# Optimization experiments

Measured on AMD Instinct MI355X. Metric: run time of the kernel, lower is better.

The kernel has to match this reference:

```python
import jax, jax.numpy as jnp
import numpy as np

B, SORB, H, L = 32768, 64, 256, 2


def setup_inputs() -> dict:
    key = jax.random.key(0)
    ks = jax.random.split(key, 11)
    s = 1.0 / np.sqrt(H)

    def u(k, shape):
        return jax.random.uniform(k, shape, jnp.float32, -s, s)

    return {
        "x": jax.random.randint(ks[0], (B, SORB), 0, 2).astype(jnp.int32),
        # PyTorch GRU params, gate order (r, z, n); layer 0 input_size=2, layer 1 input_size=H
        "w_ih0": u(ks[1], (3 * H, 2)), "w_hh0": u(ks[2], (3 * H, H)),
        "b_ih0": u(ks[3], (3 * H,)), "b_hh0": u(ks[4], (3 * H,)),
        "w_ih1": u(ks[5], (3 * H, H)), "w_hh1": u(ks[6], (3 * H, H)),
        "b_ih1": u(ks[7], (3 * H,)), "b_hh1": u(ks[8], (3 * H,)),
        "w_amp": u(ks[9], (2, H)), "b_amp": u(ks[10], (2,)),
    }


def _gru_cell(x, h, w_ih, w_hh, b_ih, b_hh):
    # PyTorch GRUCell math, gates in (r, z, n) order
    gi = x @ w_ih.T + b_ih
    gh = h @ w_hh.T + b_hh
    ir, iz, i_n = jnp.split(gi, 3, axis=-1)
    hr, hz, h_n = jnp.split(gh, 3, axis=-1)
    r = jax.nn.sigmoid(ir + hr)
    z = jax.nn.sigmoid(iz + hz)
    n = jnp.tanh(i_n + r * h_n)
    return (1.0 - z) * n + z * h


def reference(x, w_ih0, w_hh0, b_ih0, b_hh0, w_ih1, w_hh1, b_ih1, b_hh1, w_amp, b_amp):
    bits = x  # [B, SORB], values in {0,1} (equals ((+-1)+1)/2 of original input)
    nb = bits.shape[0]
    layer_params = [(w_ih0, w_hh0, b_ih0, b_hh0), (w_ih1, w_hh1, b_ih1, b_hh1)]

    def stacked(inp, h):  # h: [L, B, H]
        hs = []
        for l, (wi, wh, bi, bh) in enumerate(layer_params):
            hl = _gru_cell(inp, h[l], wi, wh, bi, bh)
            hs.append(hl)
            inp = hl
        return inp, jnp.stack(hs)

    h0 = jnp.zeros((L, nb, H), jnp.float32)
    # priming step with zero input (x0 = zeros(nbatch,1,2))
    _, h = stacked(jnp.zeros((nb, 2), jnp.float32), h0)

    def step(h, b_t):  # b_t: [B]
        onehot = jax.nn.one_hot(b_t, 2, dtype=jnp.float32)
        y, h = stacked(onehot, h)
        amp = jax.nn.softmax(y @ w_amp.T + b_amp, axis=1)  # [B, 2]
        p = jnp.sum(amp * onehot, axis=1)  # conditional prob of the sampled bit
        return h, p

    _, probs = jax.lax.scan(step, h, bits.T)  # probs: [SORB, B]
    return jnp.sqrt(jnp.prod(probs, axis=0))  # wavefunction amplitude, [B]
```

## Files before the change

kernel.cpp:

```cpp
#include <hip/hip_runtime.h>

typedef _Float16 f16;
typedef _Float16 f16x8 __attribute__((ext_vector_type(8)));
typedef float f32x4 __attribute__((ext_vector_type(4)));

#define H_    256
#define TB_   64
#define NT_   1024
#define SORB_ 64
#define SLOT_ 8192

#define MFMA16(a, b, c) __builtin_amdgcn_mfma_f32_16x16x32_f16((a), (b), (c), 0, 0, 0)
#define UNR _Pragma("unroll")

__device__ __forceinline__ float sigm(float v) {
  return __builtin_amdgcn_rcpf(1.0f + __builtin_amdgcn_exp2f(v * -1.442695040888963f));
}
__device__ __forceinline__ float tanh_fast(float v) {
  float a = fabsf(v);
  float e = __builtin_amdgcn_exp2f(a * -2.885390081777927f);
  float t = (1.0f - e) * __builtin_amdgcn_rcpf(1.0f + e);
  return copysignf(t, v);
}
__device__ __forceinline__ int lswz(int lrow, int col) {
  return lrow * H_ + (col ^ ((lrow & 7) << 3));
}

__global__ void wcvt(const float* __restrict__ a, const float* __restrict__ b,
                     const float* __restrict__ c, f16* __restrict__ o) {
  int i = blockIdx.x * 256 + threadIdx.x;
  const int n = 768 * 256;
  if (i < n) {
    o[i]         = (f16)a[i];
    o[n + i]     = (f16)b[i];
    o[2 * n + i] = (f16)c[i];
  }
}

__global__ __launch_bounds__(NT_, 4) void rnnwf(
    const int* __restrict__ x,
    const float* __restrict__ w_ih0, const float* __restrict__ b_ih0,
    const float* __restrict__ b_hh0, const float* __restrict__ b_ih1,
    const float* __restrict__ b_hh1, const float* __restrict__ w_amp,
    const float* __restrict__ b_amp, const f16* __restrict__ W16,
    float* __restrict__ out)
{
  __shared__ __align__(16) f16 hall[8 * SLOT_];
  __shared__ float wampL[512];
  __shared__ __align__(8) unsigned short bitsL[TB_ * 4];
  __shared__ unsigned long long bitsT[SORB_];

  const int tid  = threadIdx.x;
  const int wave = tid >> 6;
  const int lane = tid & 63;
  const int l15  = lane & 15;
  const int lg   = lane >> 4;
  const int lg4  = lg << 2;
  const int col  = wave * 16 + l15;
  const int rowbase = blockIdx.x * TB_;

  for (int j = tid; j < 512; j += NT_) wampL[j] = w_amp[j];
  if (tid < TB_ * 4) {
    const int* xp = x + (size_t)(rowbase + (tid >> 2)) * SORB_ + (tid & 3) * 16;
    unsigned m = 0;
    #pragma unroll
    for (int i = 0; i < 16; ++i) m |= (unsigned)(xp[i] & 1) << i;
    bitsL[tid] = (unsigned short)m;
  }
  for (int i = tid; i < 8 * SLOT_; i += NT_) hall[i] = (f16)0.f;
  __syncthreads();
  if (tid < SORB_) {
    unsigned long long mkk = 0ull;
    const int q = tid >> 4, sh = tid & 15;
    #pragma unroll 4
    for (int r = 0; r < TB_; ++r)
      mkk |= (unsigned long long)((bitsL[r * 4 + q] >> sh) & 1) << r;
    bitsT[tid] = mkk;
  }
  const int hrow = tid >> 4;
  const int t16  = tid & 15;
  const unsigned long long hmk = ((const unsigned long long*)bitsL)[hrow];

  const float baseR = b_ih0[col]       + b_hh0[col];
  const float baseZ = b_ih0[256 + col] + b_hh0[256 + col];
  const float baseN = b_ih0[512 + col];
  const float sumR0 = baseR + w_ih0[2 * col + 0],         dR = w_ih0[2 * col + 1] - w_ih0[2 * col + 0];
  const float sumZ0 = baseZ + w_ih0[2 * (256 + col) + 0], dZ = w_ih0[2 * (256 + col) + 1] - w_ih0[2 * (256 + col) + 0];
  const float sumN0 = baseN + w_ih0[2 * (512 + col) + 0], dN = w_ih0[2 * (512 + col) + 1] - w_ih0[2 * (512 + col) + 0];
  const float bhh0n_c = b_hh0[512 + col];
  const float b1r_c   = b_ih1[col]       + b_hh1[col];
  const float b1z_c   = b_ih1[256 + col] + b_hh1[256 + col];
  const float b1ni_c  = b_ih1[512 + col];
  const float b1nh_c  = b_hh1[512 + col];
  const float ba0 = b_amp[0], ba1 = b_amp[1];
  __syncthreads();

  float prob = 1.0f;
  const f16* p0base = W16 + col * 256;
  const f16* pibase = W16 + 768 * 256 + col * 256;
  const f16* phbase = W16 + 2 * 768 * 256 + col * 256;

  for (int tau = -1; tau <= 64; ++tau) {
    const int h0r = ((tau + 1) & 1) * (2 * SLOT_);
    const int h0w = (tau & 1) * (2 * SLOT_);
    const int h1r = 4 * SLOT_ + ((tau + 1) & 1) * (2 * SLOT_);
    const int h1w = 4 * SLOT_ + (tau & 1) * (2 * SLOT_);
    const bool doS = (tau < 64), doT = (tau >= 0);

    unsigned lo32 = 0u, hi32 = 0u;
    if (tau >= 0 && tau < 64) {
      unsigned long long mkk = bitsT[tau];
      lo32 = (unsigned)mkk; hi32 = (unsigned)(mkk >> 32);
    }

    f32x4 aR0[4], aZ0[4], aN0[4], tR[4], tZ[4];
    UNR for (int m = 0; m < 4; ++m) {
      aR0[m] = (f32x4){0,0,0,0}; aZ0[m] = aR0[m]; aN0[m] = aR0[m];
      tR[m] = aR0[m]; tZ[m] = aR0[m];
    }
    #pragma unroll 2
    for (int kt = 0; kt < 8; ++kt) {
      const int k0 = kt * 32 + lg * 8;
      f16x8 A0[4];
      UNR for (int m = 0; m < 4; ++m)
        A0[m] = *(const f16x8*)&hall[h0r + (m >> 1) * SLOT_ + lswz((m & 1) * 16 + l15, k0)];
      if (doS) {
        f16x8 Br = *(const f16x8*)(p0base + k0);
        f16x8 Bz = *(const f16x8*)(p0base + 65536 + k0);
        f16x8 Bn = *(const f16x8*)(p0base + 131072 + k0);
        UNR for (int m = 0; m < 4; ++m) {
          aR0[m] = MFMA16(A0[m], Br, aR0[m]);
          aZ0[m] = MFMA16(A0[m], Bz, aZ0[m]);
          aN0[m] = MFMA16(A0[m], Bn, aN0[m]);
        }
      }
      if (doT) {
        f16x8 BiR = *(const f16x8*)(pibase + k0);
        f16x8 BiZ = *(const f16x8*)(pibase + 65536 + k0);
        f16x8 BhR = *(const f16x8*)(phbase + k0);
        f16x8 BhZ = *(const f16x8*)(phbase + 65536 + k0);
        f16x8 A1[4];
        UNR for (int m = 0; m < 4; ++m)
          A1[m] = *(const f16x8*)&hall[h1r + (m >> 1) * SLOT_ + lswz((m & 1) * 16 + l15, k0)];
        UNR for (int m = 0; m < 4; ++m) {
          tR[m] = MFMA16(A0[m], BiR, tR[m]);  tR[m] = MFMA16(A1[m], BhR, tR[m]);
          tZ[m] = MFMA16(A0[m], BiZ, tZ[m]);  tZ[m] = MFMA16(A1[m], BhZ, tZ[m]);
        }
      }
    }
    f32x4 rv[4], zv[4];
    if (doT) {
      UNR for (int m = 0; m < 4; ++m)
        UNR for (int e = 0; e < 4; ++e) {
          rv[m][e] = sigm(tR[m][e] + b1r_c);
          zv[m][e] = sigm(tZ[m][e] + b1z_c);
        }
    }

    f32x4 tNi[4], tNh[4];
    UNR for (int m = 0; m < 4; ++m) { tNi[m] = (f32x4){0,0,0,0}; tNh[m] = tNi[m]; }
    if (doT) {
      #pragma unroll 2
      for (int kt = 0; kt < 8; ++kt) {
        const int k0 = kt * 32 + lg * 8;
        f16x8 BiN = *(const f16x8*)(pibase + 131072 + k0);
        f16x8 BhN = *(const f16x8*)(phbase + 131072 + k0);
        UNR for (int m = 0; m < 4; ++m) {
          f16x8 A0 = *(const f16x8*)&hall[h0r + (m >> 1) * SLOT_ + lswz((m & 1) * 16 + l15, k0)];
          f16x8 A1 = *(const f16x8*)&hall[h1r + (m >> 1) * SLOT_ + lswz((m & 1) * 16 + l15, k0)];
          tNi[m] = MFMA16(A0, BiN, tNi[m]);
          tNh[m] = MFMA16(A1, BhN, tNh[m]);
        }
      }
    }

    if (doS) {
      if (tau >= 0) {
        UNR for (int m = 0; m < 4; ++m) {
          const unsigned hsel = (m < 2) ? lo32 : hi32;
          UNR for (int e = 0; e < 4; ++e) {
            const int lrow = (m & 1) * 16 + lg4 + e;
            float fb = (float)((hsel >> ((m & 1) * 16 + lg4 + e)) & 1u);
            float giR = fmaf(fb, dR, sumR0);
            float giZ = fmaf(fb, dZ, sumZ0);
            float giN = fmaf(fb, dN, sumN0);
            float r  = sigm(aR0[m][e] + giR);
            float z  = sigm(aZ0[m][e] + giZ);
            float n  = tanh_fast(giN + r * (aN0[m][e] + bhh0n_c));
            float ho = (float)hall[h0r + (m >> 1) * SLOT_ + lswz(lrow, col)];
            hall[h0w + (m >> 1) * SLOT_ + lswz(lrow, col)] = (f16)((1.0f - z) * n + z * ho);
          }
        }
      } else {
        UNR for (int m = 0; m < 4; ++m) {
          UNR for (int e = 0; e < 4; ++e) {
            const int lrow = (m & 1) * 16 + lg4 + e;
            float r  = sigm(aR0[m][e] + baseR);
            float z  = sigm(aZ0[m][e] + baseZ);
            float n  = tanh_fast(baseN + r * (aN0[m][e] + bhh0n_c));
            float ho = (float)hall[h0r + (m >> 1) * SLOT_ + lswz(lrow, col)];
            hall[h0w + (m >> 1) * SLOT_ + lswz(lrow, col)] = (f16)((1.0f - z) * n + z * ho);
          }
        }
      }
    }
    if (doT) {
      UNR for (int m = 0; m < 4; ++m) {
        UNR for (int e = 0; e < 4; ++e) {
          const int lrow = (m & 1) * 16 + lg4 + e;
          float n  = tanh_fast(tNi[m][e] + b1ni_c + rv[m][e] * (tNh[m][e] + b1nh_c));
          float z  = zv[m][e];
          float ho = (float)hall[h1r + (m >> 1) * SLOT_ + lswz(lrow, col)];
          hall[h1w + (m >> 1) * SLOT_ + lswz(lrow, col)] = (f16)((1.0f - z) * n + z * ho);
        }
      }
    }
    if (tau >= 2) {
      const int t = tau - 2;
      float d0 = 0.f, d1 = 0.f;
      #pragma unroll
      for (int j = 0; j < 2; ++j) {
        const int k0 = t16 * 16 + j * 8;
        f16x8 hv = *(const f16x8*)&hall[h1r + (hrow >> 5) * SLOT_ + lswz(hrow & 31, k0)];
        f32x4 w0a = *(const f32x4*)&wampL[k0];
        f32x4 w0b = *(const f32x4*)&wampL[k0 + 4];
        f32x4 w1a = *(const f32x4*)&wampL[256 + k0];
        f32x4 w1b = *(const f32x4*)&wampL[256 + k0 + 4];
        #pragma unroll
        for (int i = 0; i < 4; ++i) {
          float hfa = (float)hv[i], hfb = (float)hv[4 + i];
          d0 = fmaf(hfa, w0a[i], d0); d0 = fmaf(hfb, w0b[i], d0);
          d1 = fmaf(hfa, w1a[i], d1); d1 = fmaf(hfb, w1b[i], d1);
        }
      }
      d0 += __shfl_xor(d0, 1); d0 += __shfl_xor(d0, 2);
      d0 += __shfl_xor(d0, 4); d0 += __shfl_xor(d0, 8);
      d1 += __shfl_xor(d1, 1); d1 += __shfl_xor(d1, 2);
      d1 += __shfl_xor(d1, 4); d1 += __shfl_xor(d1, 8);
      const int bit = (unsigned)(hmk >> t) & 1u;
      float diff = (d0 + ba0) - (d1 + ba1);
      if (bit) diff = -diff;
      prob *= __builtin_amdgcn_rcpf(1.0f + __builtin_amdgcn_exp2f(diff * -1.442695040888963f));
    }
    __syncthreads();
  }

  {
    const int hb = 4 * SLOT_;
    float d0 = 0.f, d1 = 0.f;
    #pragma unroll
    for (int j = 0; j < 2; ++j) {
      const int k0 = t16 * 16 + j * 8;
      f16x8 hv = *(const f16x8*)&hall[hb + (hrow >> 5) * SLOT_ + lswz(hrow & 31, k0)];
      f32x4 w0a = *(const f32x4*)&wampL[k0];
      f32x4 w0b = *(const f32x4*)&wampL[k0 + 4];
      f32x4 w1a = *(const f32x4*)&wampL[256 + k0];
      f32x4 w1b = *(const f32x4*)&wampL[256 + k0 + 4];
      #pragma unroll
      for (int i = 0; i < 4; ++i) {
        float hfa = (float)hv[i], hfb = (float)hv[4 + i];
        d0 = fmaf(hfa, w0a[i], d0); d0 = fmaf(hfb, w0b[i], d0);
        d1 = fmaf(hfa, w1a[i], d1); d1 = fmaf(hfb, w1b[i], d1);
      }
    }
    d0 += __shfl_xor(d0, 1); d0 += __shfl_xor(d0, 2);
    d0 += __shfl_xor(d0, 4); d0 += __shfl_xor(d0, 8);
    d1 += __shfl_xor(d1, 1); d1 += __shfl_xor(d1, 2);
    d1 += __shfl_xor(d1, 4); d1 += __shfl_xor(d1, 8);
    const int bit = (unsigned)(hmk >> 63) & 1u;
    float diff = (d0 + ba0) - (d1 + ba1);
    if (bit) diff = -diff;
    prob *= __builtin_amdgcn_rcpf(1.0f + __builtin_amdgcn_exp2f(diff * -1.442695040888963f));
  }

  if (t16 == 0) out[rowbase + hrow] = sqrtf(prob);
}

extern "C" void kernel_launch(void* const* d_in, const int* in_sizes, int n_in,
                              void* d_out, int out_size, void* d_ws, size_t ws_size,
                              hipStream_t stream) {
  const int*   x     = (const int*)d_in[0];
  const float* w_ih0 = (const float*)d_in[1];
  const float* w_hh0 = (const float*)d_in[2];
  const float* b_ih0 = (const float*)d_in[3];
  const float* b_hh0 = (const float*)d_in[4];
  const float* w_ih1 = (const float*)d_in[5];
  const float* w_hh1 = (const float*)d_in[6];
  const float* b_ih1 = (const float*)d_in[7];
  const float* b_hh1 = (const float*)d_in[8];
  const float* w_amp = (const float*)d_in[9];
  const float* b_amp = (const float*)d_in[10];
  (void)in_sizes; (void)n_in; (void)out_size; (void)ws_size;

  f16* W16 = (f16*)d_ws;
  hipLaunchKernelGGL(wcvt, dim3(768), dim3(256), 0, stream, w_hh0, w_ih1, w_hh1, W16);
  hipLaunchKernelGGL(rnnwf, dim3(32768 / TB_), dim3(NT_), 0, stream,
                     x, w_ih0, b_ih0, b_hh0, b_ih1, b_hh1, w_amp, b_amp, W16,
                     (float*)d_out);
}
```

Measured before the change: 5.883 ms.

## Split fused layer GEMM loops, keep previous hidden state in registers, retune LDS swizzle

```diff
diff --git a/kernel.cpp b/kernel.cpp
--- a/kernel.cpp
+++ b/kernel.cpp
@@ -2,6 +2,7 @@
 
 typedef _Float16 f16;
 typedef _Float16 f16x8 __attribute__((ext_vector_type(8)));
+typedef _Float16 f16x4 __attribute__((ext_vector_type(4)));
 typedef float f32x4 __attribute__((ext_vector_type(4)));
 
 #define H_    256
@@ -23,7 +24,7 @@
   return copysignf(t, v);
 }
 __device__ __forceinline__ int lswz(int lrow, int col) {
-  return lrow * H_ + (col ^ ((lrow & 7) << 3));
+  return lrow * H_ + (col ^ (((lrow ^ (lrow >> 2)) & 7) << 3));
 }
 
 __global__ void wcvt(const float* __restrict__ a, const float* __restrict__ b,
@@ -100,12 +101,14 @@
   const f16* pibase = W16 + 768 * 256 + col * 256;
   const f16* phbase = W16 + 2 * 768 * 256 + col * 256;
 
+  f16x4 h0p[4], h1p[4];
+  UNR for (int m = 0; m < 4; ++m) { h0p[m] = (f16x4){0,0,0,0}; h1p[m] = h0p[m]; }
+
   for (int tau = -1; tau <= 64; ++tau) {
     const int h0r = ((tau + 1) & 1) * (2 * SLOT_);
     const int h0w = (tau & 1) * (2 * SLOT_);
     const int h1r = 4 * SLOT_ + ((tau + 1) & 1) * (2 * SLOT_);
     const int h1w = 4 * SLOT_ + (tau & 1) * (2 * SLOT_);
-    const bool doS = (tau < 64), doT = (tau >= 0);
 
     unsigned lo32 = 0u, hi32 = 0u;
     if (tau >= 0 && tau < 64) {
@@ -113,53 +116,31 @@
       lo32 = (unsigned)mkk; hi32 = (unsigned)(mkk >> 32);
     }
 
-    f32x4 aR0[4], aZ0[4], aN0[4], tR[4], tZ[4];
-    UNR for (int m = 0; m < 4; ++m) {
-      aR0[m] = (f32x4){0,0,0,0}; aZ0[m] = aR0[m]; aN0[m] = aR0[m];
-      tR[m] = aR0[m]; tZ[m] = aR0[m];
-    }
-    #pragma unroll 2
-    for (int kt = 0; kt < 8; ++kt) {
-      const int k0 = kt * 32 + lg * 8;
-      f16x8 A0[4];
-      UNR for (int m = 0; m < 4; ++m)
-        A0[m] = *(const f16x8*)&hall[h0r + (m >> 1) * SLOT_ + lswz((m & 1) * 16 + l15, k0)];
-      if (doS) {
-        f16x8 Br = *(const f16x8*)(p0base + k0);
-        f16x8 Bz = *(const f16x8*)(p0base + 65536 + k0);
-        f16x8 Bn = *(const f16x8*)(p0base + 131072 + k0);
-        UNR for (int m = 0; m < 4; ++m) {
-          aR0[m] = MFMA16(A0[m], Br, aR0[m]);
-          aZ0[m] = MFMA16(A0[m], Bz, aZ0[m]);
-          aN0[m] = MFMA16(A0[m], Bn, aN0[m]);
-        }
-      }
-      if (doT) {
+    if (tau >= 0) {
+      f32x4 tR[4], tZ[4];
+      UNR for (int m = 0; m < 4; ++m) { tR[m] = (f32x4){0,0,0,0}; tZ[m] = tR[m]; }
+      #pragma unroll 2
+      for (int kt = 0; kt < 8; ++kt) {
+        const int k0 = kt * 32 + lg * 8;
         f16x8 BiR = *(const f16x8*)(pibase + k0);
         f16x8 BiZ = *(const f16x8*)(pibase + 65536 + k0);
         f16x8 BhR = *(const f16x8*)(phbase + k0);
         f16x8 BhZ = *(const f16x8*)(phbase + 65536 + k0);
-        f16x8 A1[4];
-        UNR for (int m = 0; m < 4; ++m)
-          A1[m] = *(const f16x8*)&hall[h1r + (m >> 1) * SLOT_ + lswz((m & 1) * 16 + l15, k0)];
-        UNR for (int m = 0; m < 4; ++m) {
-          tR[m] = MFMA16(A0[m], BiR, tR[m]);  tR[m] = MFMA16(A1[m], BhR, tR[m]);
-          tZ[m] = MFMA16(A0[m], BiZ, tZ[m]);  tZ[m] = MFMA16(A1[m], BhZ, tZ[m]);
-        }
-      }
-    }
-    f32x4 rv[4], zv[4];
-    if (doT) {
+        UNR for (int m = 0; m < 4; ++m) {
+          f16x8 A0 = *(const f16x8*)&hall[h0r + (m >> 1) * SLOT_ + lswz((m & 1) * 16 + l15, k0)];
+          f16x8 A1 = *(const f16x8*)&hall[h1r + (m >> 1) * SLOT_ + lswz((m & 1) * 16 + l15, k0)];
+          tR[m] = MFMA16(A0, BiR, tR[m]);  tR[m] = MFMA16(A1, BhR, tR[m]);
+          tZ[m] = MFMA16(A0, BiZ, tZ[m]);  tZ[m] = MFMA16(A1, BhZ, tZ[m]);
+        }
+      }
+      f32x4 rv[4], zv[4];
       UNR for (int m = 0; m < 4; ++m)
         UNR for (int e = 0; e < 4; ++e) {
           rv[m][e] = sigm(tR[m][e] + b1r_c);
           zv[m][e] = sigm(tZ[m][e] + b1z_c);
         }
-    }
-
-    f32x4 tNi[4], tNh[4];
-    UNR for (int m = 0; m < 4; ++m) { tNi[m] = (f32x4){0,0,0,0}; tNh[m] = tNi[m]; }
-    if (doT) {
+      f32x4 tNi[4], tNh[4];
+      UNR for (int m = 0; m < 4; ++m) { tNi[m] = (f32x4){0,0,0,0}; tNh[m] = tNi[m]; }
       #pragma unroll 2
       for (int kt = 0; kt < 8; ++kt) {
         const int k0 = kt * 32 + lg * 8;
@@ -172,9 +153,34 @@
           tNh[m] = MFMA16(A1, BhN, tNh[m]);
         }
       }
-    }
-
-    if (doS) {
+      UNR for (int m = 0; m < 4; ++m) {
+        UNR for (int e = 0; e < 4; ++e) {
+          const int lrow = (m & 1) * 16 + lg4 + e;
+          float n  = tanh_fast(tNi[m][e] + b1ni_c + rv[m][e] * (tNh[m][e] + b1nh_c));
+          float z  = zv[m][e];
+          float hn = (1.0f - z) * n + z * (float)h1p[m][e];
+          h1p[m][e] = (f16)hn;
+          hall[h1w + (m >> 1) * SLOT_ + lswz(lrow, col)] = h1p[m][e];
+        }
+      }
+    }
+
+    if (tau < 64) {
+      f32x4 aR[4], aZ[4], aN[4];
+      UNR for (int m = 0; m < 4; ++m) { aR[m] = (f32x4){0,0,0,0}; aZ[m] = aR[m]; aN[m] = aR[m]; }
+      #pragma unroll 2
+      for (int kt = 0; kt < 8; ++kt) {
+        const int k0 = kt * 32 + lg * 8;
+        f16x8 Br = *(const f16x8*)(p0base + k0);
+        f16x8 Bz = *(const f16x8*)(p0base + 65536 + k0);
+        f16x8 Bn = *(const f16x8*)(p0base + 131072 + k0);
+        UNR for (int m = 0; m < 4; ++m) {
+          f16x8 A = *(const f16x8*)&hall[h0r + (m >> 1) * SLOT_ + lswz((m & 1) * 16 + l15, k0)];
+          aR[m] = MFMA16(A, Br, aR[m]);
+          aZ[m] = MFMA16(A, Bz, aZ[m]);
+          aN[m] = MFMA16(A, Bn, aN[m]);
+        }
+      }
       if (tau >= 0) {
         UNR for (int m = 0; m < 4; ++m) {
           const unsigned hsel = (m < 2) ? lo32 : hi32;
@@ -184,37 +190,29 @@
             float giR = fmaf(fb, dR, sumR0);
             float giZ = fmaf(fb, dZ, sumZ0);
             float giN = fmaf(fb, dN, sumN0);
-            float r  = sigm(aR0[m][e] + giR);
-            float z  = sigm(aZ0[m][e] + giZ);
-            float n  = tanh_fast(giN + r * (aN0[m][e] + bhh0n_c));
-            float ho = (float)hall[h0r + (m >> 1) * SLOT_ + lswz(lrow, col)];
-            hall[h0w + (m >> 1) * SLOT_ + lswz(lrow, col)] = (f16)((1.0f - z) * n + z * ho);
+            float r  = sigm(aR[m][e] + giR);
+            float z  = sigm(aZ[m][e] + giZ);
+            float n  = tanh_fast(giN + r * (aN[m][e] + bhh0n_c));
+            float hn = (1.0f - z) * n + z * (float)h0p[m][e];
+            h0p[m][e] = (f16)hn;
+            hall[h0w + (m >> 1) * SLOT_ + lswz(lrow, col)] = h0p[m][e];
           }
         }
       } else {
         UNR for (int m = 0; m < 4; ++m) {
           UNR for (int e = 0; e < 4; ++e) {
             const int lrow = (m & 1) * 16 + lg4 + e;
-            float r  = sigm(aR0[m][e] + baseR);
-            float z  = sigm(aZ0[m][e] + baseZ);
-            float n  = tanh_fast(baseN + r * (aN0[m][e] + bhh0n_c));
-            float ho = (float)hall[h0r + (m >> 1) * SLOT_ + lswz(lrow, col)];
-            hall[h0w + (m >> 1) * SLOT_ + lswz(lrow, col)] = (f16)((1.0f - z) * n + z * ho);
+            float r  = sigm(aR[m][e] + baseR);
+            float z  = sigm(aZ[m][e] + baseZ);
+            float n  = tanh_fast(baseN + r * (aN[m][e] + bhh0n_c));
+            float hn = (1.0f - z) * n;
+            h0p[m][e] = (f16)hn;
+            hall[h0w + (m >> 1) * SLOT_ + lswz(lrow, col)] = h0p[m][e];
           }
         }
       }
     }
-    if (doT) {
-      UNR for (int m = 0; m < 4; ++m) {
-        UNR for (int e = 0; e < 4; ++e) {
-          const int lrow = (m & 1) * 16 + lg4 + e;
-          float n  = tanh_fast(tNi[m][e] + b1ni_c + rv[m][e] * (tNh[m][e] + b1nh_c));
-          float z  = zv[m][e];
-          float ho = (float)hall[h1r + (m >> 1) * SLOT_ + lswz(lrow, col)];
-          hall[h1w + (m >> 1) * SLOT_ + lswz(lrow, col)] = (f16)((1.0f - z) * n + z * ho);
-        }
-      }
-    }
+
     if (tau >= 2) {
       const int t = tau - 2;
       float d0 = 0.f, d1 = 0.f;
```

Result: faster. 5.670 ms (-3.6%).
